# Performance work log

Hardware: AMD Instinct MI355X
Metric: run time of the kernel (lower is better)

## Reference

```python
import jax, jax.numpy as jnp
import numpy as np

EMBED_DIM = 1024
NUM_HEADS = 16
HEAD_DIM = EMBED_DIM // NUM_HEADS


def setup_inputs() -> dict:
    key = jax.random.key(0)
    k_x, k_wq, k_bq, k_wo, k_bo = jax.random.split(key, 5)
    B, S, E = 4, 2048, EMBED_DIM
    lim_qkv = 1.0 / np.sqrt(E)
    lim_out = 1.0 / np.sqrt(E)
    return {
        "x": jax.random.normal(k_x, (B, S, E), dtype=jnp.float32),
        # nn.Linear stores weight [out, in]; we keep [in, out] for x @ W
        "w_qkv": jax.random.uniform(k_wq, (E, 3 * E), minval=-lim_qkv, maxval=lim_qkv, dtype=jnp.float32),
        "b_qkv": jax.random.uniform(k_bq, (3 * E,), minval=-lim_qkv, maxval=lim_qkv, dtype=jnp.float32),
        "w_out": jax.random.uniform(k_wo, (E, E), minval=-lim_out, maxval=lim_out, dtype=jnp.float32),
        "b_out": jax.random.uniform(k_bo, (E,), minval=-lim_out, maxval=lim_out, dtype=jnp.float32),
    }


def reference(x, w_qkv, b_qkv, w_out, b_out):
    B, S, E = x.shape
    H, D = NUM_HEADS, HEAD_DIM
    qkv = x @ w_qkv + b_qkv                       # [B, S, 3E]
    qkv = qkv.reshape(B, S, H, 3 * D)
    q, k, v = jnp.split(qkv, 3, axis=-1)          # each [B, S, H, D]
    scale = 1.0 / np.sqrt(D).astype(np.float32)
    scores = jnp.einsum("bshd,bthd->bhst", q, k) * scale  # [B, H, S, S]
    attn = jax.nn.softmax(scores, axis=-1)
    out = jnp.einsum("bhst,bthd->bshd", attn, v)  # [B, S, H, D]
    out = out.reshape(B, S, E)
    return out @ w_out + b_out
```

## Files before the change

### kernel.cpp

```cpp
#include <hip/hip_runtime.h>
#include <hip/hip_bf16.h>


typedef short bf16x8 __attribute__((ext_vector_type(8)));
typedef unsigned short u16x8 __attribute__((ext_vector_type(8)));
typedef short s16x4 __attribute__((ext_vector_type(4)));
typedef float f32x4 __attribute__((ext_vector_type(4)));

#define QSCALE 0.18033688011112042f

__device__ inline short f2bf(float f) {
    unsigned int u = __builtin_bit_cast(unsigned int, f);
    u += 0x7fffu + ((u >> 16) & 1u);
    return (short)(u >> 16);
}

__device__ inline unsigned int pack2bf(float a, float b) {
#if __has_builtin(__builtin_amdgcn_cvt_pk_bf16_f32)
    typedef __bf16 bf2 __attribute__((ext_vector_type(2)));
    bf2 v = __builtin_amdgcn_cvt_pk_bf16_f32(a, b);
    return __builtin_bit_cast(unsigned int, v);
#else
    return (unsigned int)(unsigned short)f2bf(a) |
           ((unsigned int)(unsigned short)f2bf(b) << 16);
#endif
}

__device__ inline float fast_exp2(float x) {
#if __has_builtin(__builtin_amdgcn_exp2f)
    return __builtin_amdgcn_exp2f(x);
#else
    float r;
    asm("v_exp_f32 %0, %1" : "=v"(r) : "v"(x));
    return r;
#endif
}

__device__ inline float fast_rcp(float x) {
#if __has_builtin(__builtin_amdgcn_rcpf)
    return __builtin_amdgcn_rcpf(x);
#else
    float r;
    asm("v_rcp_f32 %0, %1" : "=v"(r) : "v"(x));
    return r;
#endif
}

__device__ inline void gload_lds16(const short* g, short* l) {
    __builtin_amdgcn_global_load_lds(
        (const __attribute__((address_space(1))) unsigned int*)g,
        (__attribute__((address_space(3))) unsigned int*)l, 16, 0, 0);
}


__global__ __launch_bounds__(256) void cvt_bf16_kernel(const float* __restrict__ in,
                                                       short* __restrict__ out) {
    int i = blockIdx.x * 256 + threadIdx.x;
    const float4 a = *(const float4*)(in + (size_t)i * 8);
    const float4 b = *(const float4*)(in + (size_t)i * 8 + 4);
    unsigned int o0 = pack2bf(a.x, a.y), o1 = pack2bf(a.z, a.w);
    unsigned int o2 = pack2bf(b.x, b.y), o3 = pack2bf(b.z, b.w);
    uint4 o = {o0, o1, o2, o3};
    *(uint4*)(out + (size_t)i * 8) = o;
}

__global__ __launch_bounds__(256) void transpose_cvt_kernel(const float* __restrict__ in,
                                                            short* __restrict__ out,
                                                            int K, int N) {
    __shared__ float tile[32][33];
    int tx = threadIdx.x & 31, ty = threadIdx.x >> 5;
    int nt = blockIdx.x * 32, kt = blockIdx.y * 32;
    for (int i = 0; i < 4; ++i)
        tile[ty + i * 8][tx] = in[(size_t)(kt + ty + i * 8) * N + nt + tx];
    __syncthreads();
    for (int i = 0; i < 4; ++i)
        out[(size_t)(nt + ty + i * 8) * K + kt + tx] = f2bf(tile[tx][ty + i * 8]);
}

__global__ __launch_bounds__(256, 2) void gemm_qkv_kernel(
        const short* __restrict__ A, const short* __restrict__ Bt,
        const float* __restrict__ bias,
        short* __restrict__ Qg, short* __restrict__ Kg, short* __restrict__ Vtg) {
    __shared__ short As[128 * 64];
    __shared__ short Bs[128 * 64];
    const int t = threadIdx.x;
    const int w = t >> 6, lane = t & 63, r = lane & 15, q4 = lane >> 4;
    const int n0 = blockIdx.x * 128, m0 = blockIdx.y * 128;
    const int wm = (w & 1) * 64, wn = (w >> 1) * 64;

    f32x4 acc[4][4];
    for (int i = 0; i < 4; ++i)
        for (int j = 0; j < 4; ++j)
            acc[i][j] = (f32x4){0.f, 0.f, 0.f, 0.f};

    for (int kk = 0; kk < 1024; kk += 64) {
        for (int ii = 0; ii < 4; ++ii) {
            const int p = t + 256 * ii;
            const int row = p >> 3;
            const int gg = (p & 7) ^ (row & 7);
            gload_lds16(A + (size_t)(m0 + row) * 1024 + kk + gg * 8, &As[p * 8]);
            gload_lds16(Bt + (size_t)(n0 + row) * 1024 + kk + gg * 8, &Bs[p * 8]);
        }
        __syncthreads();
        for (int ko = 0; ko < 2; ++ko) {
            bf16x8 af[4], bfr[4];
            for (int i = 0; i < 4; ++i) {
                const int R = wm + i * 16 + r;
                af[i] = *(const bf16x8*)(&As[R * 64 + (((ko * 4 + q4) ^ (R & 7)) * 8)]);
            }
            for (int j = 0; j < 4; ++j) {
                const int R = wn + j * 16 + r;
                bfr[j] = *(const bf16x8*)(&Bs[R * 64 + (((ko * 4 + q4) ^ (R & 7)) * 8)]);
            }
            for (int i = 0; i < 4; ++i)
                for (int j = 0; j < 4; ++j)
                    acc[i][j] = __builtin_amdgcn_mfma_f32_16x16x32_bf16(af[i], bfr[j], acc[i][j], 0, 0, 0);
        }
        __syncthreads();
    }

    for (int i = 0; i < 4; ++i) {
        for (int j = 0; j < 4; ++j) {
            const int gn = n0 + wn + j * 16 + r;
            const int h = gn / 192;
            const int rr = gn - h * 192;
            const float bv = bias[gn];
            for (int g = 0; g < 4; ++g) {
                const int gm = m0 + wm + i * 16 + q4 * 4 + g;
                const int bb = gm >> 11;
                const int s2 = gm & 2047;
                float v = acc[i][j][g] + bv;
                const size_t bh = (size_t)(bb * 16 + h);
                if (rr < 64) {
                    Qg[(bh * 2048 + s2) * 64 + rr] = f2bf(v * QSCALE);
                } else if (rr < 128) {
                    Kg[(bh * 2048 + s2) * 64 + (rr - 64)] = f2bf(v);
                } else {
                    Vtg[(bh * 64 + (rr - 128)) * 2048 + s2] = f2bf(v);
                }
            }
        }
    }
}

__global__ __launch_bounds__(256, 4) void attn_kernel(
        const short* __restrict__ Qg, const short* __restrict__ Kg,
        const short* __restrict__ Vtg, short* __restrict__ Og) {
    __shared__ short Ks[2][64 * 64];
    __shared__ short Vs[2][64 * 64];
    __shared__ short Ps[4 * 16 * 64];
    const int t = threadIdx.x;
    const int w = t >> 6, lane = t & 63, r = lane & 15, q4 = lane >> 4;
    const int blk0 = blockIdx.x;
    const int blk = ((blk0 & 7) << 7) | (blk0 >> 3);
    const int qt = blk & 15;
    const int h = (blk >> 4) & 15;
    const int b = blk >> 8;
    const size_t bh = (size_t)b * 16 + h;
    const short* Qb = Qg + bh * 2048 * 64;
    const short* Kb = Kg + bh * 2048 * 64;
    const short* Vb = Vtg + bh * 64 * 2048;

    const int r1 = t >> 3, g1 = (t & 7) ^ (r1 & 7);
    const int r2 = 32 + (t >> 3), g2 = (t & 7) ^ (r2 & 7);
    const short* kptr1 = Kb + r1 * 64 + g1 * 8;
    const short* kptr2 = Kb + r2 * 64 + g2 * 8;
    const short* vptr1 = Vb + (size_t)r1 * 2048 + g1 * 8;
    const short* vptr2 = Vb + (size_t)r2 * 2048 + g2 * 8;

    const int swz = r & 7;
    const int ga = (q4 ^ swz) * 8;
    const int gb = ((4 + q4) ^ swz) * 8;

    bf16x8 qf[2][2];
    for (int qs = 0; qs < 2; ++qs) {
        const int qrow = qt * 128 + w * 32 + qs * 16 + r;
        qf[qs][0] = *(const bf16x8*)(Qb + (size_t)qrow * 64 + q4 * 8);
        qf[qs][1] = *(const bf16x8*)(Qb + (size_t)qrow * 64 + 32 + q4 * 8);
    }

    bf16x8 onesf;
    for (int i = 0; i < 8; ++i) onesf[i] = (short)0x3F80;

    f32x4 o[2][4], ol[2];
    for (int qs = 0; qs < 2; ++qs) {
        ol[qs] = (f32x4){0.f, 0.f, 0.f, 0.f};
        for (int nt = 0; nt < 4; ++nt) o[qs][nt] = (f32x4){0.f, 0.f, 0.f, 0.f};
    }

    const int pbase0 = w * 1024;
    const int pwb = pbase0 + r * 64 + (q4 & 1) * 4;
    const int pgq = q4 >> 1;
    const int prb = pbase0 + r * 64;

    gload_lds16(kptr1, &Ks[0][t * 8]);
    gload_lds16(kptr2, &Ks[0][(256 + t) * 8]);
    gload_lds16(vptr1, &Vs[0][t * 8]);
    gload_lds16(vptr2, &Vs[0][(256 + t) * 8]);
    __syncthreads();

    int buf = 0;
    for (int kt = 0; kt < 32; ++kt) {
        const int nb = buf ^ 1;

        if (kt + 1 < 32) {
            gload_lds16(kptr1 + (kt + 1) * 4096, &Ks[nb][t * 8]);
            gload_lds16(kptr2 + (kt + 1) * 4096, &Ks[nb][(256 + t) * 8]);
            gload_lds16(vptr1 + (kt + 1) * 64, &Vs[nb][t * 8]);
            gload_lds16(vptr2 + (kt + 1) * 64, &Vs[nb][(256 + t) * 8]);
        }

        const short* Kl = Ks[buf];
        f32x4 st[2][4];
        __builtin_amdgcn_s_setprio(1);
#pragma unroll
        for (int c = 0; c < 4; ++c) {
            const int R = (c * 16 + r) * 64;
            const bf16x8 kf0 = *(const bf16x8*)(&Kl[R + ga]);
            const bf16x8 kf1 = *(const bf16x8*)(&Kl[R + gb]);
#pragma unroll
            for (int qs = 0; qs < 2; ++qs) {
                f32x4 z = (f32x4){0.f, 0.f, 0.f, 0.f};
                z = __builtin_amdgcn_mfma_f32_16x16x32_bf16(kf0, qf[qs][0], z, 0, 0, 0);
                z = __builtin_amdgcn_mfma_f32_16x16x32_bf16(kf1, qf[qs][1], z, 0, 0, 0);
                st[qs][c] = z;
            }
        }
        __builtin_amdgcn_s_setprio(0);

        unsigned int pk[2][4][2];
#pragma unroll
        for (int qs = 0; qs < 2; ++qs)
#pragma unroll
            for (int c = 0; c < 4; ++c) {
                const float p0 = fast_exp2(st[qs][c][0]);
                const float p1 = fast_exp2(st[qs][c][1]);
                const float p2 = fast_exp2(st[qs][c][2]);
                const float p3 = fast_exp2(st[qs][c][3]);
                pk[qs][c][0] = pack2bf(p0, p1);
                pk[qs][c][1] = pack2bf(p2, p3);
            }

#pragma unroll
        for (int c = 0; c < 4; ++c) {
            uint2 u = {pk[0][c][0], pk[0][c][1]};
            *(uint2*)(&Ps[pwb + (((c * 2 + pgq) ^ swz) * 8)]) = u;
        }
        bf16x8 pf0[2];
        pf0[0] = *(const bf16x8*)(&Ps[prb + ((q4 ^ swz) * 8)]);
        pf0[1] = *(const bf16x8*)(&Ps[prb + (((4 + q4) ^ swz) * 8)]);
#pragma unroll
        for (int c = 0; c < 4; ++c) {
            uint2 u = {pk[1][c][0], pk[1][c][1]};
            *(uint2*)(&Ps[pwb + (((c * 2 + pgq) ^ swz) * 8)]) = u;
        }
        bf16x8 pf1[2];
        pf1[0] = *(const bf16x8*)(&Ps[prb + ((q4 ^ swz) * 8)]);
        pf1[1] = *(const bf16x8*)(&Ps[prb + (((4 + q4) ^ swz) * 8)]);
        asm volatile("s_waitcnt lgkmcnt(0)" ::: "memory");

        const short* Vl = Vs[buf];
        __builtin_amdgcn_s_setprio(1);
#pragma unroll
        for (int ko = 0; ko < 2; ++ko) {
            const int gk = (ko == 0) ? ga : gb;
            const bf16x8 pfa = (ko == 0) ? pf0[0] : pf0[1];
            const bf16x8 pfb = (ko == 0) ? pf1[0] : pf1[1];
            ol[0] = __builtin_amdgcn_mfma_f32_16x16x32_bf16(onesf, pfa, ol[0], 0, 0, 0);
            ol[1] = __builtin_amdgcn_mfma_f32_16x16x32_bf16(onesf, pfb, ol[1], 0, 0, 0);
#pragma unroll
            for (int nt = 0; nt < 4; ++nt) {
                const bf16x8 vf = *(const bf16x8*)(&Vl[(nt * 16 + r) * 64 + gk]);
                o[0][nt] = __builtin_amdgcn_mfma_f32_16x16x32_bf16(vf, pfa, o[0][nt], 0, 0, 0);
                o[1][nt] = __builtin_amdgcn_mfma_f32_16x16x32_bf16(vf, pfb, o[1][nt], 0, 0, 0);
            }
        }
        __builtin_amdgcn_s_setprio(0);

        __syncthreads();
        buf = nb;
    }

    for (int qs = 0; qs < 2; ++qs) {
        const float inv = fast_rcp(ol[qs][0]);
        const int srow = qt * 128 + w * 32 + qs * 16 + r;
        const size_t base = ((size_t)(b * 2048 + srow)) * 1024 + h * 64;
        for (int nt = 0; nt < 4; ++nt) {
            uint2 pko = {pack2bf(o[qs][nt][0] * inv, o[qs][nt][1] * inv),
                         pack2bf(o[qs][nt][2] * inv, o[qs][nt][3] * inv)};
            *(uint2*)(Og + base + nt * 16 + q4 * 4) = pko;
        }
    }
}

__global__ __launch_bounds__(256, 2) void gemm_out_kernel(
        const short* __restrict__ A, const short* __restrict__ Bt,
        const float* __restrict__ bias, float* __restrict__ out) {
    __shared__ short As[128 * 64];
    __shared__ short Bs[128 * 64];
    const int t = threadIdx.x;
    const int w = t >> 6, lane = t & 63, r = lane & 15, q4 = lane >> 4;
    const int n0 = blockIdx.x * 128, m0 = blockIdx.y * 128;
    const int wm = (w & 1) * 64, wn = (w >> 1) * 64;

    f32x4 acc[4][4];
    for (int i = 0; i < 4; ++i)
        for (int j = 0; j < 4; ++j)
            acc[i][j] = (f32x4){0.f, 0.f, 0.f, 0.f};

    for (int kk = 0; kk < 1024; kk += 64) {
        for (int ii = 0; ii < 4; ++ii) {
            const int p = t + 256 * ii;
            const int row = p >> 3;
            const int gg = (p & 7) ^ (row & 7);
            gload_lds16(A + (size_t)(m0 + row) * 1024 + kk + gg * 8, &As[p * 8]);
            gload_lds16(Bt + (size_t)(n0 + row) * 1024 + kk + gg * 8, &Bs[p * 8]);
        }
        __syncthreads();
        for (int ko = 0; ko < 2; ++ko) {
            bf16x8 af[4], bfr[4];
            for (int i = 0; i < 4; ++i) {
                const int R = wm + i * 16 + r;
                af[i] = *(const bf16x8*)(&As[R * 64 + (((ko * 4 + q4) ^ (R & 7)) * 8)]);
            }
            for (int j = 0; j < 4; ++j) {
                const int R = wn + j * 16 + r;
                bfr[j] = *(const bf16x8*)(&Bs[R * 64 + (((ko * 4 + q4) ^ (R & 7)) * 8)]);
            }
            for (int i = 0; i < 4; ++i)
                for (int j = 0; j < 4; ++j)
                    acc[i][j] = __builtin_amdgcn_mfma_f32_16x16x32_bf16(af[i], bfr[j], acc[i][j], 0, 0, 0);
        }
        __syncthreads();
    }

    for (int i = 0; i < 4; ++i) {
        for (int j = 0; j < 4; ++j) {
            const int gn = n0 + wn + j * 16 + r;
            const float bv = bias[gn];
            for (int g = 0; g < 4; ++g) {
                const int gm = m0 + wm + i * 16 + q4 * 4 + g;
                out[(size_t)gm * 1024 + gn] = acc[i][j][g] + bv;
            }
        }
    }
}


extern "C" void kernel_launch(void* const* d_in, const int* in_sizes, int n_in,
                              void* d_out, int out_size, void* d_ws, size_t ws_size,
                              hipStream_t stream) {
    const float* x     = (const float*)d_in[0];
    const float* w_qkv = (const float*)d_in[1];
    const float* b_qkv = (const float*)d_in[2];
    const float* w_out = (const float*)d_in[3];
    const float* b_out = (const float*)d_in[4];
    float* out = (float*)d_out;

    char* ws = (char*)d_ws;
    short* xb    = (short*)(ws);
    short* wqkvT = (short*)(ws + 16777216);
    short* woutT = (short*)(ws + 23068672);
    short* Qg    = (short*)(ws + 25165824);
    short* Kg    = (short*)(ws + 41943040);
    short* Vtg   = (short*)(ws + 58720256);
    short* attn  = xb;

    cvt_bf16_kernel<<<4096, 256, 0, stream>>>(x, xb);
    transpose_cvt_kernel<<<dim3(96, 32), 256, 0, stream>>>(w_qkv, wqkvT, 1024, 3072);
    transpose_cvt_kernel<<<dim3(32, 32), 256, 0, stream>>>(w_out, woutT, 1024, 1024);
    gemm_qkv_kernel<<<dim3(24, 64), 256, 0, stream>>>(xb, wqkvT, b_qkv, Qg, Kg, Vtg);
    attn_kernel<<<1024, 256, 0, stream>>>(Qg, Kg, Vtg, attn);
    gemm_out_kernel<<<dim3(8, 64), 256, 0, stream>>>(attn, woutT, b_out, out);
}
```

Before: 283.4 us.

## Switch attention to 32x32x16 MFMA and pass P through permlane32 swaps

Rewrites the attention inner loop to use 32x32x16 bf16 MFMA tiles instead of 16x16x32. Each wave now computes one 32-row query block. The exponentiated scores are rearranged into B-operand layout with v_permlane32_swap in registers rather than a round trip through LDS, which removes the Ps shared buffer and its write/read/waitcnt. This cuts LDS traffic and instruction count, but it depends on permlane32_swap being available and on the fragment mapping being correct. It also changes register pressure.

```diff
diff --git a/kernel.cpp b/kernel.cpp
--- a/kernel.cpp
+++ b/kernel.cpp
@@ -6,6 +6,7 @@
 typedef unsigned short u16x8 __attribute__((ext_vector_type(8)));
 typedef short s16x4 __attribute__((ext_vector_type(4)));
 typedef float f32x4 __attribute__((ext_vector_type(4)));
+typedef float f32x16 __attribute__((ext_vector_type(16)));
 
 #define QSCALE 0.18033688011112042f
 
@@ -148,9 +149,9 @@
         const short* __restrict__ Vtg, short* __restrict__ Og) {
     __shared__ short Ks[2][64 * 64];
     __shared__ short Vs[2][64 * 64];
-    __shared__ short Ps[4 * 16 * 64];
     const int t = threadIdx.x;
-    const int w = t >> 6, lane = t & 63, r = lane & 15, q4 = lane >> 4;
+    const int w = t >> 6, lane = t & 63;
+    const int l31 = lane & 31, hi = lane >> 5, lswz = lane & 7;
     const int blk0 = blockIdx.x;
     const int blk = ((blk0 & 7) << 7) | (blk0 >> 3);
     const int qt = blk & 15;
@@ -168,30 +169,19 @@
     const short* vptr1 = Vb + (size_t)r1 * 2048 + g1 * 8;
     const short* vptr2 = Vb + (size_t)r2 * 2048 + g2 * 8;
 
-    const int swz = r & 7;
-    const int ga = (q4 ^ swz) * 8;
-    const int gb = ((4 + q4) ^ swz) * 8;
-
-    bf16x8 qf[2][2];
-    for (int qs = 0; qs < 2; ++qs) {
-        const int qrow = qt * 128 + w * 32 + qs * 16 + r;
-        qf[qs][0] = *(const bf16x8*)(Qb + (size_t)qrow * 64 + q4 * 8);
-        qf[qs][1] = *(const bf16x8*)(Qb + (size_t)qrow * 64 + 32 + q4 * 8);
-    }
+    const int qbase = qt * 128 + w * 32;
+    bf16x8 qfB[4];
+#pragma unroll
+    for (int kb = 0; kb < 4; ++kb)
+        qfB[kb] = *(const bf16x8*)(Qb + (size_t)(qbase + l31) * 64 + kb * 16 + hi * 8);
 
     bf16x8 onesf;
+#pragma unroll
     for (int i = 0; i < 8; ++i) onesf[i] = (short)0x3F80;
 
-    f32x4 o[2][4], ol[2];
-    for (int qs = 0; qs < 2; ++qs) {
-        ol[qs] = (f32x4){0.f, 0.f, 0.f, 0.f};
-        for (int nt = 0; nt < 4; ++nt) o[qs][nt] = (f32x4){0.f, 0.f, 0.f, 0.f};
-    }
-
-    const int pbase0 = w * 1024;
-    const int pwb = pbase0 + r * 64 + (q4 & 1) * 4;
-    const int pgq = q4 >> 1;
-    const int prb = pbase0 + r * 64;
+    f32x16 o0, o1, ol;
+#pragma unroll
+    for (int z = 0; z < 16; ++z) { o0[z] = 0.f; o1[z] = 0.f; ol[z] = 0.f; }
 
     gload_lds16(kptr1, &Ks[0][t * 8]);
     gload_lds16(kptr2, &Ks[0][(256 + t) * 8]);
@@ -211,85 +201,60 @@
         }
 
         const short* Kl = Ks[buf];
-        f32x4 st[2][4];
-        __builtin_amdgcn_s_setprio(1);
-#pragma unroll
-        for (int c = 0; c < 4; ++c) {
-            const int R = (c * 16 + r) * 64;
-            const bf16x8 kf0 = *(const bf16x8*)(&Kl[R + ga]);
-            const bf16x8 kf1 = *(const bf16x8*)(&Kl[R + gb]);
-#pragma unroll
-            for (int qs = 0; qs < 2; ++qs) {
-                f32x4 z = (f32x4){0.f, 0.f, 0.f, 0.f};
-                z = __builtin_amdgcn_mfma_f32_16x16x32_bf16(kf0, qf[qs][0], z, 0, 0, 0);
-                z = __builtin_amdgcn_mfma_f32_16x16x32_bf16(kf1, qf[qs][1], z, 0, 0, 0);
-                st[qs][c] = z;
-            }
-        }
-        __builtin_amdgcn_s_setprio(0);
-
-        unsigned int pk[2][4][2];
-#pragma unroll
-        for (int qs = 0; qs < 2; ++qs)
-#pragma unroll
-            for (int c = 0; c < 4; ++c) {
-                const float p0 = fast_exp2(st[qs][c][0]);
-                const float p1 = fast_exp2(st[qs][c][1]);
-                const float p2 = fast_exp2(st[qs][c][2]);
-                const float p3 = fast_exp2(st[qs][c][3]);
-                pk[qs][c][0] = pack2bf(p0, p1);
-                pk[qs][c][1] = pack2bf(p2, p3);
-            }
-
-#pragma unroll
-        for (int c = 0; c < 4; ++c) {
-            uint2 u = {pk[0][c][0], pk[0][c][1]};
-            *(uint2*)(&Ps[pwb + (((c * 2 + pgq) ^ swz) * 8)]) = u;
-        }
-        bf16x8 pf0[2];
-        pf0[0] = *(const bf16x8*)(&Ps[prb + ((q4 ^ swz) * 8)]);
-        pf0[1] = *(const bf16x8*)(&Ps[prb + (((4 + q4) ^ swz) * 8)]);
-#pragma unroll
-        for (int c = 0; c < 4; ++c) {
-            uint2 u = {pk[1][c][0], pk[1][c][1]};
-            *(uint2*)(&Ps[pwb + (((c * 2 + pgq) ^ swz) * 8)]) = u;
-        }
-        bf16x8 pf1[2];
-        pf1[0] = *(const bf16x8*)(&Ps[prb + ((q4 ^ swz) * 8)]);
-        pf1[1] = *(const bf16x8*)(&Ps[prb + (((4 + q4) ^ swz) * 8)]);
-        asm volatile("s_waitcnt lgkmcnt(0)" ::: "memory");
-
         const short* Vl = Vs[buf];
-        __builtin_amdgcn_s_setprio(1);
-#pragma unroll
-        for (int ko = 0; ko < 2; ++ko) {
-            const int gk = (ko == 0) ? ga : gb;
-            const bf16x8 pfa = (ko == 0) ? pf0[0] : pf0[1];
-            const bf16x8 pfb = (ko == 0) ? pf1[0] : pf1[1];
-            ol[0] = __builtin_amdgcn_mfma_f32_16x16x32_bf16(onesf, pfa, ol[0], 0, 0, 0);
-            ol[1] = __builtin_amdgcn_mfma_f32_16x16x32_bf16(onesf, pfb, ol[1], 0, 0, 0);
-#pragma unroll
-            for (int nt = 0; nt < 4; ++nt) {
-                const bf16x8 vf = *(const bf16x8*)(&Vl[(nt * 16 + r) * 64 + gk]);
-                o[0][nt] = __builtin_amdgcn_mfma_f32_16x16x32_bf16(vf, pfa, o[0][nt], 0, 0, 0);
-                o[1][nt] = __builtin_amdgcn_mfma_f32_16x16x32_bf16(vf, pfb, o[1][nt], 0, 0, 0);
-            }
-        }
-        __builtin_amdgcn_s_setprio(0);
+#pragma unroll
+        for (int c = 0; c < 2; ++c) {
+            f32x16 st;
+#pragma unroll
+            for (int z = 0; z < 16; ++z) st[z] = 0.f;
+            __builtin_amdgcn_s_setprio(1);
+#pragma unroll
+            for (int kb = 0; kb < 4; ++kb) {
+                const bf16x8 kf = *(const bf16x8*)(
+                    &Kl[(c * 32 + l31) * 64 + (((kb * 2 + hi) ^ lswz) * 8)]);
+                st = __builtin_amdgcn_mfma_f32_32x32x16_bf16(kf, qfB[kb], st, 0, 0, 0);
+            }
+            __builtin_amdgcn_s_setprio(0);
+
+            unsigned int pkd[8];
+#pragma unroll
+            for (int m2 = 0; m2 < 8; ++m2)
+                pkd[m2] = pack2bf(fast_exp2(st[2 * m2]), fast_exp2(st[2 * m2 + 1]));
+
+#pragma unroll
+            for (int ko = 0; ko < 2; ++ko) {
+                unsigned int e0 = pkd[4 * ko + 0], e2 = pkd[4 * ko + 2];
+                unsigned int e1 = pkd[4 * ko + 1], e3 = pkd[4 * ko + 3];
+                asm("v_permlane32_swap_b32 %0, %1" : "+v"(e0), "+v"(e2));
+                asm("v_permlane32_swap_b32 %0, %1" : "+v"(e1), "+v"(e3));
+                uint4 pfu = {e0, e1, e2, e3};
+                const bf16x8 pf = __builtin_bit_cast(bf16x8, pfu);
+                __builtin_amdgcn_s_setprio(1);
+                ol = __builtin_amdgcn_mfma_f32_32x32x16_bf16(onesf, pf, ol, 0, 0, 0);
+                const bf16x8 vf0 = *(const bf16x8*)(
+                    &Vl[l31 * 64 + (((c * 4 + ko * 2 + hi) ^ lswz) * 8)]);
+                o0 = __builtin_amdgcn_mfma_f32_32x32x16_bf16(vf0, pf, o0, 0, 0, 0);
+                const bf16x8 vf1 = *(const bf16x8*)(
+                    &Vl[(32 + l31) * 64 + (((c * 4 + ko * 2 + hi) ^ lswz) * 8)]);
+                o1 = __builtin_amdgcn_mfma_f32_32x32x16_bf16(vf1, pf, o1, 0, 0, 0);
+                __builtin_amdgcn_s_setprio(0);
+            }
+        }
 
         __syncthreads();
         buf = nb;
     }
 
-    for (int qs = 0; qs < 2; ++qs) {
-        const float inv = fast_rcp(ol[qs][0]);
-        const int srow = qt * 128 + w * 32 + qs * 16 + r;
-        const size_t base = ((size_t)(b * 2048 + srow)) * 1024 + h * 64;
-        for (int nt = 0; nt < 4; ++nt) {
-            uint2 pko = {pack2bf(o[qs][nt][0] * inv, o[qs][nt][1] * inv),
-                         pack2bf(o[qs][nt][2] * inv, o[qs][nt][3] * inv)};
-            *(uint2*)(Og + base + nt * 16 + q4 * 4) = pko;
-        }
+    const float inv = fast_rcp(ol[0]);
+    const size_t rowbase = ((size_t)(b * 2048 + qbase + l31)) * 1024 + h * 64 + hi * 4;
+#pragma unroll
+    for (int bq = 0; bq < 4; ++bq) {
+        uint2 pk0 = {pack2bf(o0[4 * bq + 0] * inv, o0[4 * bq + 1] * inv),
+                     pack2bf(o0[4 * bq + 2] * inv, o0[4 * bq + 3] * inv)};
+        *(uint2*)(Og + rowbase + 8 * bq) = pk0;
+        uint2 pk1 = {pack2bf(o1[4 * bq + 0] * inv, o1[4 * bq + 1] * inv),
+                     pack2bf(o1[4 * bq + 2] * inv, o1[4 * bq + 3] * inv)};
+        *(uint2*)(Og + rowbase + 32 + 8 * bq) = pk1;
     }
 }
 
```

New measurement: 290.6 us. +2.6%, slower.

## Pipeline GEMMs with triple-buffered LDS, larger tiles, and merge prep kernels

Applied to the files above, without the earlier changes.

The two projection GEMMs are rewritten to use 512-thread blocks computing 256x128 tiles with a 32-wide K step. Global-to-LDS loads go through a three-stage ring buffer with explicit vmcnt waits and raw barriers, so loads for future stages overlap the MFMA work instead of stalling on a full sync each iteration. The three preprocessing launches (x conversion and two weight transposes) are folded into one kernel to cut launch overhead. The tradeoffs are more LDS per block, hand-managed wait counts that must stay correct, and fewer blocks for the out-projection grid.

```diff
diff --git a/kernel.cpp b/kernel.cpp
--- a/kernel.cpp
+++ b/kernel.cpp
@@ -52,24 +52,27 @@
         (__attribute__((address_space(3))) unsigned int*)l, 16, 0, 0);
 }
 
-
-__global__ __launch_bounds__(256) void cvt_bf16_kernel(const float* __restrict__ in,
-                                                       short* __restrict__ out) {
-    int i = blockIdx.x * 256 + threadIdx.x;
-    const float4 a = *(const float4*)(in + (size_t)i * 8);
-    const float4 b = *(const float4*)(in + (size_t)i * 8 + 4);
-    unsigned int o0 = pack2bf(a.x, a.y), o1 = pack2bf(a.z, a.w);
-    unsigned int o2 = pack2bf(b.x, b.y), o3 = pack2bf(b.z, b.w);
-    uint4 o = {o0, o1, o2, o3};
-    *(uint4*)(out + (size_t)i * 8) = o;
-}
-
-__global__ __launch_bounds__(256) void transpose_cvt_kernel(const float* __restrict__ in,
-                                                            short* __restrict__ out,
-                                                            int K, int N) {
+__global__ __launch_bounds__(256) void prep_kernel(
+        const float* __restrict__ x, short* __restrict__ xb,
+        const float* __restrict__ w_qkv, short* __restrict__ wqkvT,
+        const float* __restrict__ w_out, short* __restrict__ woutT) {
+    const int bid = blockIdx.x;
+    if (bid < 4096) {
+        int i = bid * 256 + threadIdx.x;
+        const float4 a = *(const float4*)(x + (size_t)i * 8);
+        const float4 b = *(const float4*)(x + (size_t)i * 8 + 4);
+        uint4 o = {pack2bf(a.x, a.y), pack2bf(a.z, a.w),
+                   pack2bf(b.x, b.y), pack2bf(b.z, b.w)};
+        *(uint4*)(xb + (size_t)i * 8) = o;
+        return;
+    }
     __shared__ float tile[32][33];
+    const float* in; short* out; int N, bx, by;
+    if (bid < 7168) { int k = bid - 4096; bx = k % 96; by = k / 96; in = w_qkv; out = wqkvT; N = 3072; }
+    else            { int k = bid - 7168; bx = k & 31; by = k >> 5; in = w_out; out = woutT; N = 1024; }
+    const int K = 1024;
     int tx = threadIdx.x & 31, ty = threadIdx.x >> 5;
-    int nt = blockIdx.x * 32, kt = blockIdx.y * 32;
+    int nt = bx * 32, kt = by * 32;
     for (int i = 0; i < 4; ++i)
         tile[ty + i * 8][tx] = in[(size_t)(kt + ty + i * 8) * N + nt + tx];
     __syncthreads();
@@ -77,47 +80,74 @@
         out[(size_t)(nt + ty + i * 8) * K + kt + tx] = f2bf(tile[tx][ty + i * 8]);
 }
 
-__global__ __launch_bounds__(256, 2) void gemm_qkv_kernel(
+#define GEMM_STAGE(As_, Bs_, Agl_, Btgl_, s_, kk_) do {                          \
+    _Pragma("unroll")                                                            \
+    for (int ii = 0; ii < 2; ++ii) {                                             \
+        const int p = t + 512 * ii; const int row = p >> 2;                      \
+        const int gg = (p & 3) ^ (row & 3);                                      \
+        gload_lds16(Agl_ + (size_t)(m0 + row) * 1024 + (kk_) + gg * 8,           \
+                    &As_[s_][p * 8]);                                            \
+    }                                                                            \
+    {                                                                            \
+        const int p = t; const int row = p >> 2;                                 \
+        const int gg = (p & 3) ^ (row & 3);                                      \
+        gload_lds16(Btgl_ + (size_t)(n0 + row) * 1024 + (kk_) + gg * 8,          \
+                    &Bs_[s_][p * 8]);                                            \
+    } } while (0)
+
+#define GEMM_MAINLOOP(As_, Bs_, Agl_, Btgl_)                                     \
+    GEMM_STAGE(As_, Bs_, Agl_, Btgl_, 0, 0);                                     \
+    GEMM_STAGE(As_, Bs_, Agl_, Btgl_, 1, 32);                                    \
+    asm volatile("s_waitcnt vmcnt(3)" ::: "memory");                             \
+    __builtin_amdgcn_s_barrier();                                                \
+    int cur = 0;                                                                 \
+    _Pragma("unroll 1")                                                          \
+    for (int ts = 0; ts < 32; ++ts) {                                            \
+        const int nx2 = (cur == 0) ? 2 : cur - 1;                 \
+        if (ts + 2 < 32) GEMM_STAGE(As_, Bs_, Agl_, Btgl_, nx2, (ts + 2) * 32);  \
+        const short* Asl = As_[cur];                                             \
+        const short* Bsl = Bs_[cur];                                             \
+        bf16x8 af[4], bfr[4];                                                    \
+        _Pragma("unroll")                                                        \
+        for (int i = 0; i < 4; ++i) {                                            \
+            const int R = wm + i * 16 + r;                                       \
+            af[i] = *(const bf16x8*)(&Asl[R * 32 + (((q4 ^ (R & 3)) * 8))]);     \
+        }                                                                        \
+        _Pragma("unroll")                                                        \
+        for (int j = 0; j < 4; ++j) {                                            \
+            const int R = wn + j * 16 + r;                                       \
+            bfr[j] = *(const bf16x8*)(&Bsl[R * 32 + (((q4 ^ (R & 3)) * 8))]);    \
+        }                                                                        \
+        __builtin_amdgcn_s_setprio(1);                                           \
+        _Pragma("unroll")                                                        \
+        for (int i = 0; i < 4; ++i)                                              \
+            _Pragma("unroll")                                                    \
+            for (int j = 0; j < 4; ++j)                                          \
+                acc[i][j] = __builtin_amdgcn_mfma_f32_16x16x32_bf16(af[i], bfr[j], acc[i][j], 0, 0, 0); \
+        __builtin_amdgcn_s_setprio(0);                                           \
+        if (ts + 2 < 32) { asm volatile("s_waitcnt vmcnt(3)" ::: "memory"); }    \
+        else             { asm volatile("s_waitcnt vmcnt(0)" ::: "memory"); }    \
+        __builtin_amdgcn_s_barrier();                                            \
+        cur = (cur == 2) ? 0 : cur + 1;                                          \
+    }
+
+__global__ __launch_bounds__(512, 4) void gemm_qkv_kernel(
         const short* __restrict__ A, const short* __restrict__ Bt,
         const float* __restrict__ bias,
         short* __restrict__ Qg, short* __restrict__ Kg, short* __restrict__ Vtg) {
-    __shared__ short As[128 * 64];
-    __shared__ short Bs[128 * 64];
+    __shared__ __align__(16) short As[3][256 * 32];
+    __shared__ __align__(16) short Bs[3][128 * 32];
     const int t = threadIdx.x;
     const int w = t >> 6, lane = t & 63, r = lane & 15, q4 = lane >> 4;
-    const int n0 = blockIdx.x * 128, m0 = blockIdx.y * 128;
-    const int wm = (w & 1) * 64, wn = (w >> 1) * 64;
+    const int wm = (w >> 1) * 64, wn = (w & 1) * 64;
+    const int n0 = blockIdx.x * 128, m0 = blockIdx.y * 256;
 
     f32x4 acc[4][4];
     for (int i = 0; i < 4; ++i)
         for (int j = 0; j < 4; ++j)
             acc[i][j] = (f32x4){0.f, 0.f, 0.f, 0.f};
 
-    for (int kk = 0; kk < 1024; kk += 64) {
-        for (int ii = 0; ii < 4; ++ii) {
-            const int p = t + 256 * ii;
-            const int row = p >> 3;
-            const int gg = (p & 7) ^ (row & 7);
-            gload_lds16(A + (size_t)(m0 + row) * 1024 + kk + gg * 8, &As[p * 8]);
-            gload_lds16(Bt + (size_t)(n0 + row) * 1024 + kk + gg * 8, &Bs[p * 8]);
-        }
-        __syncthreads();
-        for (int ko = 0; ko < 2; ++ko) {
-            bf16x8 af[4], bfr[4];
-            for (int i = 0; i < 4; ++i) {
-                const int R = wm + i * 16 + r;
-                af[i] = *(const bf16x8*)(&As[R * 64 + (((ko * 4 + q4) ^ (R & 7)) * 8)]);
-            }
-            for (int j = 0; j < 4; ++j) {
-                const int R = wn + j * 16 + r;
-                bfr[j] = *(const bf16x8*)(&Bs[R * 64 + (((ko * 4 + q4) ^ (R & 7)) * 8)]);
-            }
-            for (int i = 0; i < 4; ++i)
-                for (int j = 0; j < 4; ++j)
-                    acc[i][j] = __builtin_amdgcn_mfma_f32_16x16x32_bf16(af[i], bfr[j], acc[i][j], 0, 0, 0);
-        }
-        __syncthreads();
-    }
+    GEMM_MAINLOOP(As, Bs, A, Bt)
 
     for (int i = 0; i < 4; ++i) {
         for (int j = 0; j < 4; ++j) {
@@ -293,46 +323,22 @@
     }
 }
 
-__global__ __launch_bounds__(256, 2) void gemm_out_kernel(
+__global__ __launch_bounds__(512, 4) void gemm_out_kernel(
         const short* __restrict__ A, const short* __restrict__ Bt,
         const float* __restrict__ bias, float* __restrict__ out) {
-    __shared__ short As[128 * 64];
-    __shared__ short Bs[128 * 64];
+    __shared__ __align__(16) short As[3][256 * 32];
+    __shared__ __align__(16) short Bs[3][128 * 32];
     const int t = threadIdx.x;
     const int w = t >> 6, lane = t & 63, r = lane & 15, q4 = lane >> 4;
-    const int n0 = blockIdx.x * 128, m0 = blockIdx.y * 128;
-    const int wm = (w & 1) * 64, wn = (w >> 1) * 64;
+    const int wm = (w >> 1) * 64, wn = (w & 1) * 64;
+    const int n0 = blockIdx.x * 128, m0 = blockIdx.y * 256;
 
     f32x4 acc[4][4];
     for (int i = 0; i < 4; ++i)
         for (int j = 0; j < 4; ++j)
             acc[i][j] = (f32x4){0.f, 0.f, 0.f, 0.f};
 
-    for (int kk = 0; kk < 1024; kk += 64) {
-        for (int ii = 0; ii < 4; ++ii) {
-            const int p = t + 256 * ii;
-            const int row = p >> 3;
-            const int gg = (p & 7) ^ (row & 7);
-            gload_lds16(A + (size_t)(m0 + row) * 1024 + kk + gg * 8, &As[p * 8]);
-            gload_lds16(Bt + (size_t)(n0 + row) * 1024 + kk + gg * 8, &Bs[p * 8]);
-        }
-        __syncthreads();
-        for (int ko = 0; ko < 2; ++ko) {
-            bf16x8 af[4], bfr[4];
-            for (int i = 0; i < 4; ++i) {
-                const int R = wm + i * 16 + r;
-                af[i] = *(const bf16x8*)(&As[R * 64 + (((ko * 4 + q4) ^ (R & 7)) * 8)]);
-            }
-            for (int j = 0; j < 4; ++j) {
-                const int R = wn + j * 16 + r;
-                bfr[j] = *(const bf16x8*)(&Bs[R * 64 + (((ko * 4 + q4) ^ (R & 7)) * 8)]);
-            }
-            for (int i = 0; i < 4; ++i)
-                for (int j = 0; j < 4; ++j)
-                    acc[i][j] = __builtin_amdgcn_mfma_f32_16x16x32_bf16(af[i], bfr[j], acc[i][j], 0, 0, 0);
-        }
-        __syncthreads();
-    }
+    GEMM_MAINLOOP(As, Bs, A, Bt)
 
     for (int i = 0; i < 4; ++i) {
         for (int j = 0; j < 4; ++j) {
@@ -366,10 +372,8 @@
     short* Vtg   = (short*)(ws + 58720256);
     short* attn  = xb;
 
-    cvt_bf16_kernel<<<4096, 256, 0, stream>>>(x, xb);
-    transpose_cvt_kernel<<<dim3(96, 32), 256, 0, stream>>>(w_qkv, wqkvT, 1024, 3072);
-    transpose_cvt_kernel<<<dim3(32, 32), 256, 0, stream>>>(w_out, woutT, 1024, 1024);
-    gemm_qkv_kernel<<<dim3(24, 64), 256, 0, stream>>>(xb, wqkvT, b_qkv, Qg, Kg, Vtg);
+    prep_kernel<<<8192, 256, 0, stream>>>(x, xb, w_qkv, wqkvT, w_out, woutT);
+    gemm_qkv_kernel<<<dim3(24, 32), 512, 0, stream>>>(xb, wqkvT, b_qkv, Qg, Kg, Vtg);
     attn_kernel<<<1024, 256, 0, stream>>>(Qg, Kg, Vtg, attn);
-    gemm_out_kernel<<<dim3(8, 64), 256, 0, stream>>>(attn, woutT, b_out, out);
-}
+    gemm_out_kernel<<<dim3(8, 32), 512, 0, stream>>>(attn, woutT, b_out, out);
+}
```

After: 300.0 us. 1.06x slower.

## Merge prep kernels into one launch and vectorize GEMM epilogue stores via swapped MFMA operands

Applied to the files above, without the earlier changes.

Combines the x conversion and both weight transpose-convert kernels into one prep kernel that dispatches on block index, removing two launches. In both GEMMs the MFMA operands are swapped so each lane holds four consecutive output columns instead of four rows. This lets the epilogues use float4 bias loads and packed uint2/float4 stores for Q, K and the output, replacing scalar strided writes. The V-transposed stores remain scalar and now land in four different rows per lane.

```diff
diff --git a/kernel.cpp b/kernel.cpp
--- a/kernel.cpp
+++ b/kernel.cpp
@@ -52,24 +52,27 @@
         (__attribute__((address_space(3))) unsigned int*)l, 16, 0, 0);
 }
 
-
-__global__ __launch_bounds__(256) void cvt_bf16_kernel(const float* __restrict__ in,
-                                                       short* __restrict__ out) {
-    int i = blockIdx.x * 256 + threadIdx.x;
-    const float4 a = *(const float4*)(in + (size_t)i * 8);
-    const float4 b = *(const float4*)(in + (size_t)i * 8 + 4);
-    unsigned int o0 = pack2bf(a.x, a.y), o1 = pack2bf(a.z, a.w);
-    unsigned int o2 = pack2bf(b.x, b.y), o3 = pack2bf(b.z, b.w);
-    uint4 o = {o0, o1, o2, o3};
-    *(uint4*)(out + (size_t)i * 8) = o;
-}
-
-__global__ __launch_bounds__(256) void transpose_cvt_kernel(const float* __restrict__ in,
-                                                            short* __restrict__ out,
-                                                            int K, int N) {
+__global__ __launch_bounds__(256) void prep_kernel(
+        const float* __restrict__ x, short* __restrict__ xb,
+        const float* __restrict__ w_qkv, short* __restrict__ wqkvT,
+        const float* __restrict__ w_out, short* __restrict__ woutT) {
+    const int bid = blockIdx.x;
+    if (bid < 4096) {
+        int i = bid * 256 + threadIdx.x;
+        const float4 a = *(const float4*)(x + (size_t)i * 8);
+        const float4 b = *(const float4*)(x + (size_t)i * 8 + 4);
+        uint4 o = {pack2bf(a.x, a.y), pack2bf(a.z, a.w),
+                   pack2bf(b.x, b.y), pack2bf(b.z, b.w)};
+        *(uint4*)(xb + (size_t)i * 8) = o;
+        return;
+    }
     __shared__ float tile[32][33];
+    const float* in; short* out; int N, bx, by;
+    if (bid < 7168) { int k = bid - 4096; bx = k % 96; by = k / 96; in = w_qkv; out = wqkvT; N = 3072; }
+    else            { int k = bid - 7168; bx = k & 31; by = k >> 5; in = w_out; out = woutT; N = 1024; }
+    const int K = 1024;
     int tx = threadIdx.x & 31, ty = threadIdx.x >> 5;
-    int nt = blockIdx.x * 32, kt = blockIdx.y * 32;
+    int nt = bx * 32, kt = by * 32;
     for (int i = 0; i < 4; ++i)
         tile[ty + i * 8][tx] = in[(size_t)(kt + ty + i * 8) * N + nt + tx];
     __syncthreads();
@@ -114,30 +117,38 @@
             }
             for (int i = 0; i < 4; ++i)
                 for (int j = 0; j < 4; ++j)
-                    acc[i][j] = __builtin_amdgcn_mfma_f32_16x16x32_bf16(af[i], bfr[j], acc[i][j], 0, 0, 0);
+                    acc[i][j] = __builtin_amdgcn_mfma_f32_16x16x32_bf16(bfr[j], af[i], acc[i][j], 0, 0, 0);
         }
         __syncthreads();
     }
 
     for (int i = 0; i < 4; ++i) {
+        const int gm = m0 + wm + i * 16 + r;
+        const int bb = gm >> 11;
+        const int s2 = gm & 2047;
         for (int j = 0; j < 4; ++j) {
-            const int gn = n0 + wn + j * 16 + r;
-            const int h = gn / 192;
-            const int rr = gn - h * 192;
-            const float bv = bias[gn];
-            for (int g = 0; g < 4; ++g) {
-                const int gm = m0 + wm + i * 16 + q4 * 4 + g;
-                const int bb = gm >> 11;
-                const int s2 = gm & 2047;
-                float v = acc[i][j][g] + bv;
-                const size_t bh = (size_t)(bb * 16 + h);
-                if (rr < 64) {
-                    Qg[(bh * 2048 + s2) * 64 + rr] = f2bf(v * QSCALE);
-                } else if (rr < 128) {
-                    Kg[(bh * 2048 + s2) * 64 + (rr - 64)] = f2bf(v);
-                } else {
-                    Vtg[(bh * 64 + (rr - 128)) * 2048 + s2] = f2bf(v);
-                }
+            const int gnb = n0 + wn + j * 16 + q4 * 4;
+            const int h = gnb / 192;
+            const int rr = gnb - h * 192;
+            const float4 bv = *(const float4*)(bias + gnb);
+            const float v0 = acc[i][j][0] + bv.x;
+            const float v1 = acc[i][j][1] + bv.y;
+            const float v2 = acc[i][j][2] + bv.z;
+            const float v3 = acc[i][j][3] + bv.w;
+            const size_t bh = (size_t)(bb * 16 + h);
+            if (rr < 64) {
+                uint2 p = {pack2bf(v0 * QSCALE, v1 * QSCALE),
+                           pack2bf(v2 * QSCALE, v3 * QSCALE)};
+                *(uint2*)(Qg + (bh * 2048 + s2) * 64 + rr) = p;
+            } else if (rr < 128) {
+                uint2 p = {pack2bf(v0, v1), pack2bf(v2, v3)};
+                *(uint2*)(Kg + (bh * 2048 + s2) * 64 + (rr - 64)) = p;
+            } else {
+                const int d0 = rr - 128;
+                Vtg[(bh * 64 + d0 + 0) * 2048 + s2] = f2bf(v0);
+                Vtg[(bh * 64 + d0 + 1) * 2048 + s2] = f2bf(v1);
+                Vtg[(bh * 64 + d0 + 2) * 2048 + s2] = f2bf(v2);
+                Vtg[(bh * 64 + d0 + 3) * 2048 + s2] = f2bf(v3);
             }
         }
     }
@@ -329,19 +340,19 @@
             }
             for (int i = 0; i < 4; ++i)
                 for (int j = 0; j < 4; ++j)
-                    acc[i][j] = __builtin_amdgcn_mfma_f32_16x16x32_bf16(af[i], bfr[j], acc[i][j], 0, 0, 0);
+                    acc[i][j] = __builtin_amdgcn_mfma_f32_16x16x32_bf16(bfr[j], af[i], acc[i][j], 0, 0, 0);
         }
         __syncthreads();
     }
 
     for (int i = 0; i < 4; ++i) {
+        const int gm = m0 + wm + i * 16 + r;
         for (int j = 0; j < 4; ++j) {
-            const int gn = n0 + wn + j * 16 + r;
-            const float bv = bias[gn];
-            for (int g = 0; g < 4; ++g) {
-                const int gm = m0 + wm + i * 16 + q4 * 4 + g;
-                out[(size_t)gm * 1024 + gn] = acc[i][j][g] + bv;
-            }
+            const int gnb = n0 + wn + j * 16 + q4 * 4;
+            const float4 bv = *(const float4*)(bias + gnb);
+            float4 v = {acc[i][j][0] + bv.x, acc[i][j][1] + bv.y,
+                        acc[i][j][2] + bv.z, acc[i][j][3] + bv.w};
+            *(float4*)(out + (size_t)gm * 1024 + gnb) = v;
         }
     }
 }
@@ -366,9 +377,7 @@
     short* Vtg   = (short*)(ws + 58720256);
     short* attn  = xb;
 
-    cvt_bf16_kernel<<<4096, 256, 0, stream>>>(x, xb);
-    transpose_cvt_kernel<<<dim3(96, 32), 256, 0, stream>>>(w_qkv, wqkvT, 1024, 3072);
-    transpose_cvt_kernel<<<dim3(32, 32), 256, 0, stream>>>(w_out, woutT, 1024, 1024);
+    prep_kernel<<<8192, 256, 0, stream>>>(x, xb, w_qkv, wqkvT, w_out, woutT);
     gemm_qkv_kernel<<<dim3(24, 64), 256, 0, stream>>>(xb, wqkvT, b_qkv, Qg, Kg, Vtg);
     attn_kernel<<<1024, 256, 0, stream>>>(Qg, Kg, Vtg, attn);
     gemm_out_kernel<<<dim3(8, 64), 256, 0, stream>>>(attn, woutT, b_out, out);
```

New measurement: 282.1 us. Within noise of the previous version (-0.4%).
